# Optimization experiments

Hardware: AMD Instinct MI355X
Metric: run time of the kernel (lower is better)

## Reference

```python
import jax, jax.numpy as jnp
import numpy as np

DIM = 512
NUM_HEADS = 8
HEAD_DIM = DIM // NUM_HEADS
SCALE = HEAD_DIM ** -0.5


def setup_inputs() -> dict:
    key = jax.random.key(0)
    k_x, k_wqkv, k_bqkv, k_wp, k_bp = jax.random.split(key, 5)
    x = jax.random.normal(k_x, (2, 4096, DIM), dtype=jnp.float32)
    s = DIM ** -0.5
    W_qkv = jax.random.normal(k_wqkv, (DIM, 3 * DIM), dtype=jnp.float32) * s
    b_qkv = jax.random.normal(k_bqkv, (3 * DIM,), dtype=jnp.float32) * 0.02
    W_proj = jax.random.normal(k_wp, (DIM, DIM), dtype=jnp.float32) * s
    b_proj = jax.random.normal(k_bp, (DIM,), dtype=jnp.float32) * 0.02
    return {"x": x, "W_qkv": W_qkv, "b_qkv": b_qkv, "W_proj": W_proj, "b_proj": b_proj}


def reference(x, W_qkv, b_qkv, W_proj, b_proj):
    B, S, D = x.shape
    H, Hd = NUM_HEADS, HEAD_DIM
    qkv = x @ W_qkv + b_qkv                      # [B, S, 3D]
    qkv = qkv.reshape(B, S, 3, H, Hd)
    q, k, v = jnp.moveaxis(qkv, 2, 0)            # each [B, S, H, Hd]
    # scores: [B, H, S, S] (explicit, matching the original non-fused impl)
    attn = jnp.einsum('bshd,bthd->bhst', q, k) * SCALE
    attn = jax.nn.softmax(attn, axis=-1)
    out = jnp.einsum('bhst,bthd->bshd', attn, v) # [B, S, H, Hd]
    out = out.reshape(B, S, D)
    return out @ W_proj + b_proj
```

## Files before the change

### kernel.cpp

```cpp
#include <hip/hip_runtime.h>
#include <hip/hip_bf16.h>
#include <stdint.h>

typedef __attribute__((ext_vector_type(8))) short bf16x8;
typedef __attribute__((ext_vector_type(4))) float f32x4;
typedef __attribute__((ext_vector_type(16))) float f32x16;
typedef __attribute__((ext_vector_type(4))) int i32x4;

__device__ __forceinline__ short f2bf(float f) {
  uint32_t u = __builtin_bit_cast(uint32_t, f);
  u = u + 0x7FFFu + ((u >> 16) & 1u);
  return (short)(u >> 16);
}


__global__ __launch_bounds__(256) void convert_x_kernel(const float* __restrict__ x,
                                                        short* __restrict__ xb) {
  int i = (blockIdx.x * 256 + threadIdx.x) * 8;
  float4 v0 = *(const float4*)(x + i);
  float4 v1 = *(const float4*)(x + i + 4);
  uint32_t p0 = (uint16_t)f2bf(v0.x) | ((uint32_t)(uint16_t)f2bf(v0.y) << 16);
  uint32_t p1 = (uint16_t)f2bf(v0.z) | ((uint32_t)(uint16_t)f2bf(v0.w) << 16);
  uint32_t p2 = (uint16_t)f2bf(v1.x) | ((uint32_t)(uint16_t)f2bf(v1.y) << 16);
  uint32_t p3 = (uint16_t)f2bf(v1.z) | ((uint32_t)(uint16_t)f2bf(v1.w) << 16);
  i32x4 o = {(int)p0, (int)p1, (int)p2, (int)p3};
  *(i32x4*)(xb + i) = o;
}

__global__ __launch_bounds__(256) void transpose_w_kernel(const float* __restrict__ W,
                                                          short* __restrict__ Wt, int N,
                                                          int nTilesN) {
  __shared__ short Ts[64 * 66];
  const int t = threadIdx.x;
  const int n0 = (blockIdx.x % nTilesN) * 64;
  const int k0 = (blockIdx.x / nTilesN) * 64;
#pragma unroll
  for (int j = 0; j < 16; j++) {
    int e = j * 256 + t;
    int k = e >> 6, n = e & 63;
    Ts[k * 66 + n] = f2bf(W[(size_t)(k0 + k) * N + n0 + n]);
  }
  __syncthreads();
#pragma unroll
  for (int j = 0; j < 16; j++) {
    int e = j * 256 + t;
    int n = e >> 6, k = e & 63;
    Wt[(size_t)(n0 + n) * 512 + k0 + k] = Ts[k * 66 + n];
  }
}


__global__ __launch_bounds__(256) void gemm_qkv_kernel(const short* __restrict__ A,
                                                       const short* __restrict__ Bt,
                                                       const float* __restrict__ bias,
                                                       short* __restrict__ Qb,
                                                       short* __restrict__ Kb,
                                                       short* __restrict__ Vt) {
  __shared__ short Al[128 * 32];
  __shared__ short Bl[128 * 32];
  const int tid = threadIdx.x;
  const int bm = (blockIdx.x & 63) << 7;
  const int bn = (blockIdx.x >> 6) << 7;
  const int lane = tid & 63;
  const int wv = tid >> 6;
  const int wm = (wv >> 1) * 64, wn = (wv & 1) * 64;
  const int lr = lane & 15, lg = lane >> 4;

  f32x4 acc[4][4];
#pragma unroll
  for (int i = 0; i < 4; i++)
#pragma unroll
    for (int j = 0; j < 4; j++) acc[i][j] = (f32x4){0.f, 0.f, 0.f, 0.f};

  for (int k0 = 0; k0 < 512; k0 += 32) {
    __syncthreads();
#pragma unroll
    for (int i = 0; i < 2; ++i) {
      int c = tid + i * 256;
      int row = c >> 2, coff = (c & 3) * 8;
      __builtin_amdgcn_global_load_lds(
          (const __attribute__((address_space(1))) void*)(A + (size_t)(bm + row) * 512 + k0 + coff),
          (__attribute__((address_space(3))) void*)(&Al[c * 8]), 16, 0, 0);
      __builtin_amdgcn_global_load_lds(
          (const __attribute__((address_space(1))) void*)(Bt + (size_t)(bn + row) * 512 + k0 + coff),
          (__attribute__((address_space(3))) void*)(&Bl[c * 8]), 16, 0, 0);
    }
    __syncthreads();
    bf16x8 a[4], b[4];
#pragma unroll
    for (int mi = 0; mi < 4; mi++) a[mi] = *(const bf16x8*)(&Al[(wm + mi * 16 + lr) * 32 + lg * 8]);
#pragma unroll
    for (int ni = 0; ni < 4; ni++) b[ni] = *(const bf16x8*)(&Bl[(wn + ni * 16 + lr) * 32 + lg * 8]);
#pragma unroll
    for (int mi = 0; mi < 4; mi++)
#pragma unroll
      for (int ni = 0; ni < 4; ni++)
        acc[mi][ni] = __builtin_amdgcn_mfma_f32_16x16x32_bf16(a[mi], b[ni], acc[mi][ni], 0, 0, 0);
  }

#pragma unroll
  for (int ni = 0; ni < 4; ni++) {
    int n = bn + wn + ni * 16 + lr;
    float bv = bias[n];
    int three = n >> 9, hn = n & 511;
    int h = hn >> 6, d = hn & 63;
#pragma unroll
    for (int mi = 0; mi < 4; mi++) {
#pragma unroll
      for (int r = 0; r < 4; r++) {
        int m = bm + wm + mi * 16 + lg * 4 + r;
        int bb = m >> 12, s = m & 4095;
        float v = acc[mi][ni][r] + bv;
        int bh = bb * 8 + h;
        if (three == 0) {
          Qb[((size_t)bh * 4096 + s) * 64 + d] = f2bf(v * 0.125f);
        } else if (three == 1) {
          Kb[((size_t)bh * 4096 + s) * 64 + d] = f2bf(v);
        } else {
          Vt[((size_t)bh * 64 + d) * 4096 + s] = f2bf(v);
        }
      }
    }
  }
}


__global__ __launch_bounds__(256, 2) void attn_kernel(const short* __restrict__ Qb,
                                                      const short* __restrict__ Kb,
                                                      const short* __restrict__ Vt,
                                                      short* __restrict__ Ob) {
  __shared__ short Kl[2][64 * 64];
  __shared__ short Vl[2][64 * 64];

  const int tid = threadIdx.x;
  const int lane = tid & 63;
  const int wv = tid >> 6;
  const int q5 = lane & 31, h = lane >> 5;
  const int b = blockIdx.x;
  const int qt = (b >> 3) & 31;
  const int bh = (b & 7) | ((b >> 8) << 3);

  const int qrow = qt * 128 + wv * 32 + q5;
  const short* Qrow = Qb + ((size_t)bh * 4096 + qrow) * 64;
  bf16x8 qf[4];
#pragma unroll
  for (int c = 0; c < 4; c++) qf[c] = *(const bf16x8*)(Qrow + c * 16 + h * 8);

  float m_run = -1e30f, l_run = 0.f;
  f32x16 oA, oB;
#pragma unroll
  for (int r = 0; r < 16; r++) { oA[r] = 0.f; oB[r] = 0.f; }

  const size_t kgbase = (size_t)bh * 4096 * 64;
  const size_t vgbase = (size_t)bh * 64 * 4096;

  const int srow = lane >> 3;
  const int schunk = ((lane & 7) ^ srow) * 8;
  const int li0 = wv * 2;

  auto stage = [&](int buf, int kb_) {
#pragma unroll
    for (int i = 0; i < 2; i++) {
      const int li = li0 + i;
      const int row = li * 8 + srow;
      __builtin_amdgcn_global_load_lds(
          (const __attribute__((address_space(1))) void*)(Kb + kgbase + (size_t)(kb_ + row) * 64 + schunk),
          (__attribute__((address_space(3))) void*)(&Kl[buf][li * 512]), 16, 0, 0);
      __builtin_amdgcn_global_load_lds(
          (const __attribute__((address_space(1))) void*)(Vt + vgbase + (size_t)row * 4096 + kb_ + schunk),
          (__attribute__((address_space(3))) void*)(&Vl[buf][li * 512]), 16, 0, 0);
    }
  };

  stage(0, 0);
  __syncthreads();
  int cur = 0;

  const int vsw = (q5 & 7) << 4;

  for (int kb = 0; kb < 4096; kb += 64) {
    if (kb + 64 < 4096) stage(cur ^ 1, kb + 64);
    const short* Kc = &Kl[cur][0];
    const short* Vc = &Vl[cur][0];

#pragma unroll
    for (int ks = 0; ks < 2; ks++) {
      f32x16 sc;
#pragma unroll
      for (int r = 0; r < 16; r++) sc[r] = 0.f;
      {
        const int krow = ks * 32 + q5;
        const char* kbase = (const char*)Kc + krow * 128;
        const int ksw = (krow & 7) << 4;
#pragma unroll
        for (int c = 0; c < 4; c++) {
          bf16x8 kf = *(const bf16x8*)(kbase + ((((c << 1) + h) << 4) ^ ksw));
          sc = __builtin_amdgcn_mfma_f32_32x32x16_bf16(kf, qf[c], sc, 0, 0, 0);
        }
      }

      float pm = sc[0];
#pragma unroll
      for (int r = 1; r < 16; r++) pm = fmaxf(pm, sc[r]);
      pm = fmaxf(pm, __shfl_xor(pm, 32, 64));

      if (!__all(pm <= m_run + 8.0f)) {
        float nm = fmaxf(m_run, pm);
        float fac = exp2f((m_run - nm) * 1.44269504f);
        m_run = nm;
        l_run *= fac;
#pragma unroll
        for (int r = 0; r < 16; r++) {
          const int qm = (r & 3) + 8 * (r >> 2);
          float fr = __shfl(fac, qm + (h << 2), 64);
          oA[r] *= fr;
          oB[r] *= fr;
        }
      }

      const float mb = m_run * 1.44269504f;
      float p[16];
      float ls = 0.f;
#pragma unroll
      for (int r = 0; r < 16; r++) {
        p[r] = exp2f(__builtin_fmaf(sc[r], 1.44269504f, -mb));
        ls += p[r];
      }
      ls += __shfl_xor(ls, 32, 64);
      l_run += ls;

      uint32_t w0, w1, w2, w3, w4, w5, w6, w7;
      asm("v_cvt_pk_bf16_f32 %0, %1, %2" : "=v"(w0) : "v"(p[0]), "v"(p[1]));
      asm("v_cvt_pk_bf16_f32 %0, %1, %2" : "=v"(w1) : "v"(p[2]), "v"(p[3]));
      asm("v_cvt_pk_bf16_f32 %0, %1, %2" : "=v"(w2) : "v"(p[4]), "v"(p[5]));
      asm("v_cvt_pk_bf16_f32 %0, %1, %2" : "=v"(w3) : "v"(p[6]), "v"(p[7]));
      asm("v_cvt_pk_bf16_f32 %0, %1, %2" : "=v"(w4) : "v"(p[8]), "v"(p[9]));
      asm("v_cvt_pk_bf16_f32 %0, %1, %2" : "=v"(w5) : "v"(p[10]), "v"(p[11]));
      asm("v_cvt_pk_bf16_f32 %0, %1, %2" : "=v"(w6) : "v"(p[12]), "v"(p[13]));
      asm("v_cvt_pk_bf16_f32 %0, %1, %2" : "=v"(w7) : "v"(p[14]), "v"(p[15]));
      uint32_t e0 = (uint32_t)__shfl_xor((int)(h ? w0 : w2), 32, 64);
      uint32_t e1 = (uint32_t)__shfl_xor((int)(h ? w1 : w3), 32, 64);
      uint32_t e2 = (uint32_t)__shfl_xor((int)(h ? w4 : w6), 32, 64);
      uint32_t e3 = (uint32_t)__shfl_xor((int)(h ? w5 : w7), 32, 64);
      i32x4 fa0 = {(int)(h ? e0 : w0), (int)(h ? e1 : w1), (int)(h ? w2 : e0), (int)(h ? w3 : e1)};
      i32x4 fa1 = {(int)(h ? e2 : w4), (int)(h ? e3 : w5), (int)(h ? w6 : e2), (int)(h ? w7 : e3)};
      bf16x8 pa0 = __builtin_bit_cast(bf16x8, fa0);
      bf16x8 pa1 = __builtin_bit_cast(bf16x8, fa1);

      {
        const char* vb0 = (const char*)Vc + q5 * 128;
        const char* vb1 = vb0 + 32 * 128;
        const int c0 = ((ks * 4 + h) << 4) ^ vsw;
        const int c1 = ((ks * 4 + 2 + h) << 4) ^ vsw;
        bf16x8 va00 = *(const bf16x8*)(vb0 + c0);
        bf16x8 va01 = *(const bf16x8*)(vb0 + c1);
        bf16x8 va10 = *(const bf16x8*)(vb1 + c0);
        bf16x8 va11 = *(const bf16x8*)(vb1 + c1);
        oA = __builtin_amdgcn_mfma_f32_32x32x16_bf16(pa0, va00, oA, 0, 0, 0);
        oA = __builtin_amdgcn_mfma_f32_32x32x16_bf16(pa1, va01, oA, 0, 0, 0);
        oB = __builtin_amdgcn_mfma_f32_32x32x16_bf16(pa0, va10, oB, 0, 0, 0);
        oB = __builtin_amdgcn_mfma_f32_32x32x16_bf16(pa1, va11, oB, 0, 0, 0);
      }
    }

    __syncthreads();
    cur ^= 1;
  }

  const int bb = bh >> 3, hh = bh & 7;
  float linv = 1.0f / l_run;
#pragma unroll
  for (int r = 0; r < 16; r++) {
    const int qm = (r & 3) + 8 * (r >> 2);
    float li = __shfl(linv, qm + (h << 2), 64);
    int orow = qt * 128 + wv * 32 + qm + 4 * h;
    size_t rowb = ((size_t)bb * 4096 + orow) * 512 + hh * 64;
    Ob[rowb + q5] = f2bf(oA[r] * li);
    Ob[rowb + 32 + q5] = f2bf(oB[r] * li);
  }
}


__global__ __launch_bounds__(256) void gemm_proj_kernel(const short* __restrict__ A,
                                                        const short* __restrict__ Bt,
                                                        const float* __restrict__ bias,
                                                        float* __restrict__ out) {
  __shared__ short Al[128 * 32];
  __shared__ short Bl[128 * 32];
  const int tid = threadIdx.x;
  const int bm = (blockIdx.x & 63) << 7;
  const int bn = (blockIdx.x >> 6) << 7;
  const int lane = tid & 63;
  const int wv = tid >> 6;
  const int wm = (wv >> 1) * 64, wn = (wv & 1) * 64;
  const int lr = lane & 15, lg = lane >> 4;

  f32x4 acc[4][4];
#pragma unroll
  for (int i = 0; i < 4; i++)
#pragma unroll
    for (int j = 0; j < 4; j++) acc[i][j] = (f32x4){0.f, 0.f, 0.f, 0.f};

  for (int k0 = 0; k0 < 512; k0 += 32) {
    __syncthreads();
#pragma unroll
    for (int i = 0; i < 2; ++i) {
      int c = tid + i * 256;
      int row = c >> 2, coff = (c & 3) * 8;
      __builtin_amdgcn_global_load_lds(
          (const __attribute__((address_space(1))) void*)(A + (size_t)(bm + row) * 512 + k0 + coff),
          (__attribute__((address_space(3))) void*)(&Al[c * 8]), 16, 0, 0);
      __builtin_amdgcn_global_load_lds(
          (const __attribute__((address_space(1))) void*)(Bt + (size_t)(bn + row) * 512 + k0 + coff),
          (__attribute__((address_space(3))) void*)(&Bl[c * 8]), 16, 0, 0);
    }
    __syncthreads();
    bf16x8 a[4], b[4];
#pragma unroll
    for (int mi = 0; mi < 4; mi++) a[mi] = *(const bf16x8*)(&Al[(wm + mi * 16 + lr) * 32 + lg * 8]);
#pragma unroll
    for (int ni = 0; ni < 4; ni++) b[ni] = *(const bf16x8*)(&Bl[(wn + ni * 16 + lr) * 32 + lg * 8]);
#pragma unroll
    for (int mi = 0; mi < 4; mi++)
#pragma unroll
      for (int ni = 0; ni < 4; ni++)
        acc[mi][ni] = __builtin_amdgcn_mfma_f32_16x16x32_bf16(a[mi], b[ni], acc[mi][ni], 0, 0, 0);
  }

#pragma unroll
  for (int ni = 0; ni < 4; ni++) {
    int n = bn + wn + ni * 16 + lr;
    float bv = bias[n];
#pragma unroll
    for (int mi = 0; mi < 4; mi++) {
#pragma unroll
      for (int r = 0; r < 4; r++) {
        int m = bm + wm + mi * 16 + lg * 4 + r;
        out[(size_t)m * 512 + n] = acc[mi][ni][r] + bv;
      }
    }
  }
}


extern "C" void kernel_launch(void* const* d_in, const int* in_sizes, int n_in,
                              void* d_out, int out_size, void* d_ws, size_t ws_size,
                              hipStream_t stream) {
  const float* x = (const float*)d_in[0];
  const float* Wqkv = (const float*)d_in[1];
  const float* bqkv = (const float*)d_in[2];
  const float* Wproj = (const float*)d_in[3];
  const float* bproj = (const float*)d_in[4];
  float* out = (float*)d_out;

  char* ws = (char*)d_ws;
  short* xb  = (short*)(ws);
  short* Wqt = (short*)(ws + 8388608);
  short* Wpt = (short*)(ws + 9961472);
  short* Qb  = (short*)(ws + 10485760);
  short* Kb  = (short*)(ws + 18874368);
  short* Vt  = (short*)(ws + 27262976);
  short* Ob  = (short*)(ws + 35651584);

  convert_x_kernel<<<2048, 256, 0, stream>>>(x, xb);
  transpose_w_kernel<<<192, 256, 0, stream>>>(Wqkv, Wqt, 1536, 24);
  transpose_w_kernel<<<64, 256, 0, stream>>>(Wproj, Wpt, 512, 8);
  gemm_qkv_kernel<<<768, 256, 0, stream>>>(xb, Wqt, bqkv, Qb, Kb, Vt);
  attn_kernel<<<512, 256, 0, stream>>>(Qb, Kb, Vt, Ob);
  gemm_proj_kernel<<<256, 256, 0, stream>>>(Ob, Wpt, bproj, out);
}
```

Before: 256.2 us.

## Split attention KV range across two wave groups per block and merge partials

```diff
diff --git a/kernel.cpp b/kernel.cpp
--- a/kernel.cpp
+++ b/kernel.cpp
@@ -125,22 +125,26 @@
 }
 
 
-__global__ __launch_bounds__(256, 2) void attn_kernel(const short* __restrict__ Qb,
+__global__ __launch_bounds__(512, 4) void attn_kernel(const short* __restrict__ Qb,
                                                       const short* __restrict__ Kb,
                                                       const short* __restrict__ Vt,
                                                       short* __restrict__ Ob) {
-  __shared__ short Kl[2][64 * 64];
-  __shared__ short Vl[2][64 * 64];
+  __shared__ short Kl[2][2][64 * 64];
+  __shared__ short Vl[2][2][64 * 64];
+  __shared__ float Ml[2][4][64];
+  __shared__ float Ll[4][64];
 
   const int tid = threadIdx.x;
   const int lane = tid & 63;
   const int wv = tid >> 6;
+  const int wg = wv & 3;
+  const int grp = wv >> 2;
   const int q5 = lane & 31, h = lane >> 5;
   const int b = blockIdx.x;
   const int qt = (b >> 3) & 31;
   const int bh = (b & 7) | ((b >> 8) << 3);
 
-  const int qrow = qt * 128 + wv * 32 + q5;
+  const int qrow = qt * 128 + wg * 32 + q5;
   const short* Qrow = Qb + ((size_t)bh * 4096 + qrow) * 64;
   bf16x8 qf[4];
 #pragma unroll
@@ -151,24 +155,24 @@
 #pragma unroll
   for (int r = 0; r < 16; r++) { oA[r] = 0.f; oB[r] = 0.f; }
 
-  const size_t kgbase = (size_t)bh * 4096 * 64;
-  const size_t vgbase = (size_t)bh * 64 * 4096;
+  const size_t kgbase = (size_t)bh * 4096 * 64 + (size_t)grp * 2048 * 64;
+  const size_t vgbase = (size_t)bh * 64 * 4096 + (size_t)grp * 2048;
 
   const int srow = lane >> 3;
-  const int schunk = ((lane & 7) ^ srow) * 8;
-  const int li0 = wv * 2;
+  const int li0 = wg * 2;
 
   auto stage = [&](int buf, int kb_) {
 #pragma unroll
     for (int i = 0; i < 2; i++) {
       const int li = li0 + i;
       const int row = li * 8 + srow;
+      const int schunk = (((lane & 7) ^ srow ^ (li & 3)) << 3);
       __builtin_amdgcn_global_load_lds(
           (const __attribute__((address_space(1))) void*)(Kb + kgbase + (size_t)(kb_ + row) * 64 + schunk),
-          (__attribute__((address_space(3))) void*)(&Kl[buf][li * 512]), 16, 0, 0);
+          (__attribute__((address_space(3))) void*)(&Kl[grp][buf][li * 512]), 16, 0, 0);
       __builtin_amdgcn_global_load_lds(
           (const __attribute__((address_space(1))) void*)(Vt + vgbase + (size_t)row * 4096 + kb_ + schunk),
-          (__attribute__((address_space(3))) void*)(&Vl[buf][li * 512]), 16, 0, 0);
+          (__attribute__((address_space(3))) void*)(&Vl[grp][buf][li * 512]), 16, 0, 0);
     }
   };
 
@@ -176,12 +180,12 @@
   __syncthreads();
   int cur = 0;
 
-  const int vsw = (q5 & 7) << 4;
-
-  for (int kb = 0; kb < 4096; kb += 64) {
-    if (kb + 64 < 4096) stage(cur ^ 1, kb + 64);
-    const short* Kc = &Kl[cur][0];
-    const short* Vc = &Vl[cur][0];
+  const int rsw = (((q5 & 7) ^ (q5 >> 3)) << 4);
+
+  for (int kb = 0; kb < 2048; kb += 64) {
+    if (kb + 64 < 2048) stage(cur ^ 1, kb + 64);
+    const short* Kc = &Kl[grp][cur][0];
+    const short* Vc = &Vl[grp][cur][0];
 
 #pragma unroll
     for (int ks = 0; ks < 2; ks++) {
@@ -189,12 +193,10 @@
 #pragma unroll
       for (int r = 0; r < 16; r++) sc[r] = 0.f;
       {
-        const int krow = ks * 32 + q5;
-        const char* kbase = (const char*)Kc + krow * 128;
-        const int ksw = (krow & 7) << 4;
+        const char* kbase = (const char*)Kc + (ks * 32 + q5) * 128;
 #pragma unroll
         for (int c = 0; c < 4; c++) {
-          bf16x8 kf = *(const bf16x8*)(kbase + ((((c << 1) + h) << 4) ^ ksw));
+          bf16x8 kf = *(const bf16x8*)(kbase + ((((c << 1) + h) << 4) ^ rsw));
           sc = __builtin_amdgcn_mfma_f32_32x32x16_bf16(kf, qf[c], sc, 0, 0, 0);
         }
       }
@@ -250,8 +252,8 @@
       {
         const char* vb0 = (const char*)Vc + q5 * 128;
         const char* vb1 = vb0 + 32 * 128;
-        const int c0 = ((ks * 4 + h) << 4) ^ vsw;
-        const int c1 = ((ks * 4 + 2 + h) << 4) ^ vsw;
+        const int c0 = (((ks * 4 + h) << 4)) ^ rsw;
+        const int c1 = (((ks * 4 + 2 + h) << 4)) ^ rsw;
         bf16x8 va00 = *(const bf16x8*)(vb0 + c0);
         bf16x8 va01 = *(const bf16x8*)(vb0 + c1);
         bf16x8 va10 = *(const bf16x8*)(vb1 + c0);
@@ -267,16 +269,40 @@
     cur ^= 1;
   }
 
-  const int bb = bh >> 3, hh = bh & 7;
-  float linv = 1.0f / l_run;
-#pragma unroll
-  for (int r = 0; r < 16; r++) {
-    const int qm = (r & 3) + 8 * (r >> 2);
-    float li = __shfl(linv, qm + (h << 2), 64);
-    int orow = qt * 128 + wv * 32 + qm + 4 * h;
-    size_t rowb = ((size_t)bb * 4096 + orow) * 512 + hh * 64;
-    Ob[rowb + q5] = f2bf(oA[r] * li);
-    Ob[rowb + 32 + q5] = f2bf(oB[r] * li);
+  Ml[grp][wg][lane] = m_run;
+  __syncthreads();
+  const float mp = Ml[grp ^ 1][wg][lane];
+  const float M = fmaxf(m_run, mp);
+  const float fac = exp2f((m_run - M) * 1.44269504f);
+  const float lsc = l_run * fac;
+  float* Om = (float*)&Kl[0][0][0];
+  if (grp == 1) {
+    Ll[wg][lane] = lsc;
+#pragma unroll
+    for (int r = 0; r < 16; r++) {
+      const int qm = (r & 3) + 8 * (r >> 2);
+      float fr = __shfl(fac, qm + (h << 2), 64);
+      Om[(wg * 32 + r) * 64 + lane] = oA[r] * fr;
+      Om[(wg * 32 + 16 + r) * 64 + lane] = oB[r] * fr;
+    }
+  }
+  __syncthreads();
+  if (grp == 0) {
+    const float l_tot = lsc + Ll[wg][lane];
+    const float linv = 1.0f / l_tot;
+    const int bb = bh >> 3, hh = bh & 7;
+#pragma unroll
+    for (int r = 0; r < 16; r++) {
+      const int qm = (r & 3) + 8 * (r >> 2);
+      float fr = __shfl(fac, qm + (h << 2), 64);
+      float li = __shfl(linv, qm + (h << 2), 64);
+      float vA = oA[r] * fr + Om[(wg * 32 + r) * 64 + lane];
+      float vB = oB[r] * fr + Om[(wg * 32 + 16 + r) * 64 + lane];
+      int orow = qt * 128 + wg * 32 + qm + 4 * h;
+      size_t rowb = ((size_t)bb * 4096 + orow) * 512 + hh * 64;
+      Ob[rowb + q5] = f2bf(vA * li);
+      Ob[rowb + 32 + q5] = f2bf(vB * li);
+    }
   }
 }
 
@@ -366,6 +392,6 @@
   transpose_w_kernel<<<192, 256, 0, stream>>>(Wqkv, Wqt, 1536, 24);
   transpose_w_kernel<<<64, 256, 0, stream>>>(Wproj, Wpt, 512, 8);
   gemm_qkv_kernel<<<768, 256, 0, stream>>>(xb, Wqt, bqkv, Qb, Kb, Vt);
-  attn_kernel<<<512, 256, 0, stream>>>(Qb, Kb, Vt, Ob);
+  attn_kernel<<<512, 512, 0, stream>>>(Qb, Kb, Vt, Ob);
   gemm_proj_kernel<<<256, 256, 0, stream>>>(Ob, Wpt, bproj, out);
 }
```

New measurement: 236.6 us. 7.6% less time.
